# Kernel tuning notes

Measured on AMD Instinct MI355X. Metric: run time of the kernel, lower is better.

## Reference

```python
import jax, jax.numpy as jnp
import numpy as np

N, E = 50000, 800000
IN, H, C = 256, 8, 32  # heads=8, hidden_dim=32 -> out dim 256
NEG_SLOPE = 0.2
EPS = 1e-5


def setup_inputs() -> dict:
    key = jax.random.key(0)
    ks = jax.random.split(key, 6)
    x = jax.random.normal(ks[0], (N, IN), jnp.float32)
    edge_index = jax.random.randint(ks[1], (2, E), 0, N, dtype=jnp.int32)
    W = jax.random.normal(ks[2], (IN, H * C), jnp.float32) / np.sqrt(IN).astype(np.float32)
    att_src = jax.random.normal(ks[3], (H, C), jnp.float32) * 0.1
    att_dst = jax.random.normal(ks[4], (H, C), jnp.float32) * 0.1
    bias = jnp.zeros((H * C,), jnp.float32)
    gamma = jnp.ones((H * C,), jnp.float32)
    beta = jnp.zeros((H * C,), jnp.float32)
    return {"x": x, "edge_index": edge_index, "W": W, "att_src": att_src,
            "att_dst": att_dst, "bias": bias, "gamma": gamma, "beta": beta}


def reference(x, edge_index, W, att_src, att_dst, bias, gamma, beta):
    n = x.shape[0]
    # Linear projection -> per-head features [N, H, C]
    xl = (x @ W).reshape(n, H, C)
    # Per-node attention half-logits [N, H]
    a_src = jnp.einsum('nhc,hc->nh', xl, att_src)
    a_dst = jnp.einsum('nhc,hc->nh', xl, att_dst)
    # Add self loops (PyG GATConv default)
    loops = jnp.arange(n, dtype=edge_index.dtype)
    src = jnp.concatenate([edge_index[0], loops])  # [E+N]
    dst = jnp.concatenate([edge_index[1], loops])
    # Edge attention logits + segment softmax over destination neighborhoods
    logits = jax.nn.leaky_relu(a_src[src] + a_dst[dst], NEG_SLOPE)  # [E+N, H]
    seg_max = jax.ops.segment_max(logits, dst, num_segments=n)
    ex = jnp.exp(logits - seg_max[dst])
    denom = jax.ops.segment_sum(ex, dst, num_segments=n)
    alpha = ex / denom[dst]  # [E+N, H]
    # Weighted scatter-aggregation of source features
    msgs = xl[src] * alpha[:, :, None]  # [E+N, H, C]
    out = jax.ops.segment_sum(msgs, dst, num_segments=n).reshape(n, H * C) + bias
    # LayerNorm over feature dim
    mu = jnp.mean(out, axis=-1, keepdims=True)
    var = jnp.var(out, axis=-1, keepdims=True)
    return (out - mu) / jnp.sqrt(var + EPS) * gamma + beta
```

## Files before the change

### kernel.cpp

```cpp
#include <hip/hip_runtime.h>
#include <math.h>

#define NEG 0.2f
#define LNEPS 1e-5f

typedef __attribute__((ext_vector_type(8))) short bf16x8;
typedef __attribute__((ext_vector_type(4))) float f32x4;

__device__ __forceinline__ float lrelu(float x){ return x > 0.f ? x : NEG*x; }

__device__ __forceinline__ short f2b(float f){
  unsigned u = __float_as_uint(f);
  unsigned r = u + 0x7fffu + ((u >> 16) & 1u);
  return (short)(r >> 16);
}
__device__ __forceinline__ float b2f(unsigned short u){
  return __uint_as_float(((unsigned)u) << 16);
}

__global__ __launch_bounds__(256) void wt_k(const float* __restrict__ W,
                                            unsigned short* __restrict__ WT){
  int idx = blockIdx.x*256 + threadIdx.x;
  int k = idx >> 8, c = idx & 255;
  WT[c*256 + k] = (unsigned short)f2b(W[idx]);
}

__device__ __forceinline__ void load_half(float4 nx[8], const float* p){
  #pragma unroll
  for (int s=0;s<4;s++){
    nx[2*s]   = *(const float4*)(p + s*32);
    nx[2*s+1] = *(const float4*)(p + s*32 + 4);
  }
}
__device__ __forceinline__ void cvt_half(bf16x8 af[4], const float4 nx[8]){
  #pragma unroll
  for (int s=0;s<4;s++){
    af[s][0]=f2b(nx[2*s].x);   af[s][1]=f2b(nx[2*s].y);
    af[s][2]=f2b(nx[2*s].z);   af[s][3]=f2b(nx[2*s].w);
    af[s][4]=f2b(nx[2*s+1].x); af[s][5]=f2b(nx[2*s+1].y);
    af[s][6]=f2b(nx[2*s+1].z); af[s][7]=f2b(nx[2*s+1].w);
  }
}

__global__ __launch_bounds__(256, 2) void mfma_gemm_k(const float* __restrict__ A,
    const unsigned short* __restrict__ WT, unsigned short* __restrict__ Cb,
    const float* __restrict__ att_src, const float* __restrict__ att_dst,
    float* __restrict__ a_src, float* __restrict__ a_dst, int M, int nTiles){
  int w   = threadIdx.x >> 6;
  int l   = threadIdx.x & 63;
  int l15 = l & 15;
  int kg  = l >> 4;
  int colbase = w*64;

  bf16x8 bfr[4][8];
  #pragma unroll
  for (int j=0;j<4;j++){
    const unsigned short* bp = WT + (size_t)(colbase + j*16 + l15)*256 + kg*8;
    #pragma unroll
    for (int ks=0;ks<8;ks++) bfr[j][ks] = *(const bf16x8*)(bp + ks*32);
  }
  float as_r[4], ad_r[4];
  #pragma unroll
  for (int j=0;j<4;j++){
    as_r[j] = att_src[colbase + j*16 + l15];
    ad_r[j] = att_dst[colbase + j*16 + l15];
  }

  int t = blockIdx.x;
  if (t >= nTiles) return;
  int row0 = t*16 + l15;
  const float* ap = A + (size_t)(row0 < M ? row0 : M-1)*256 + kg*8;
  float4 nx[8];
  load_half(nx, ap);

  while (t < nTiles){
    f32x4 acc[4];
    #pragma unroll
    for (int j=0;j<4;j++) acc[j] = (f32x4){0.f,0.f,0.f,0.f};
    bf16x8 af[4];

    cvt_half(af, nx);
    load_half(nx, ap + 128);
    #pragma unroll
    for (int s=0;s<4;s++)
      #pragma unroll
      for (int j=0;j<4;j++)
        acc[j] = __builtin_amdgcn_mfma_f32_16x16x32_bf16(af[s], bfr[j][s], acc[j], 0, 0, 0);

    int tn = t + gridDim.x;
    int rown = tn < nTiles ? tn*16 + l15 : row0;
    const float* apn = A + (size_t)(rown < M ? rown : M-1)*256 + kg*8;

    cvt_half(af, nx);
    load_half(nx, apn);
    #pragma unroll
    for (int s=0;s<4;s++)
      #pragma unroll
      for (int j=0;j<4;j++)
        acc[j] = __builtin_amdgcn_mfma_f32_16x16x32_bf16(af[s], bfr[j][4+s], acc[j], 0, 0, 0);

    int orow_base = t*16 + kg*4;
    #pragma unroll
    for (int j=0;j<4;j++)
      #pragma unroll
      for (int rr=0;rr<4;rr++){
        int orow = orow_base + rr;
        if (orow < M) Cb[(size_t)orow*256 + colbase + j*16 + l15] = (unsigned short)f2b(acc[j][rr]);
      }
    #pragma unroll
    for (int rr=0;rr<4;rr++){
      float p0s = acc[0][rr]*as_r[0] + acc[1][rr]*as_r[1];
      float p0d = acc[0][rr]*ad_r[0] + acc[1][rr]*ad_r[1];
      float p1s = acc[2][rr]*as_r[2] + acc[3][rr]*as_r[3];
      float p1d = acc[2][rr]*ad_r[2] + acc[3][rr]*ad_r[3];
      #pragma unroll
      for (int m=1;m<16;m<<=1){
        p0s += __shfl_xor(p0s,m); p0d += __shfl_xor(p0d,m);
        p1s += __shfl_xor(p1s,m); p1d += __shfl_xor(p1d,m);
      }
      int orow = orow_base + rr;
      if (l15==0 && orow < M){
        a_src[(size_t)orow*8 + 2*w]   = p0s;
        a_dst[(size_t)orow*8 + 2*w]   = p0d;
        a_src[(size_t)orow*8 + 2*w+1] = p1s;
        a_dst[(size_t)orow*8 + 2*w+1] = p1d;
      }
    }
    t = tn; row0 = rown; ap = apn;
  }
}

__global__ void deg_k(const int* __restrict__ dst, int* __restrict__ deg, int E){
  int e = blockIdx.x*blockDim.x+threadIdx.x;
  if (e<E) atomicAdd(&deg[dst[e]],1);
}

__global__ __launch_bounds__(1024) void scan1_k(const int* __restrict__ deg,
                                                int* __restrict__ off,
                                                int* __restrict__ bsum, int n){
  __shared__ int wsum[16];
  int tid=threadIdx.x, lane=tid&63, wid=tid>>6;
  int i = blockIdx.x*1024 + tid;
  int v = (i<n)?deg[i]:0;
  int x = v;
  #pragma unroll
  for (int s=1;s<64;s<<=1){ int t2=__shfl_up(x,s); if (lane>=s) x+=t2; }
  if (lane==63) wsum[wid]=x;
  __syncthreads();
  if (tid<16){
    int y=wsum[tid];
    #pragma unroll
    for (int s=1;s<16;s<<=1){ int t2=__shfl_up(y,s); if (tid>=s) y+=t2; }
    wsum[tid]=y;
  }
  __syncthreads();
  int prefix=(wid? wsum[wid-1]:0);
  if (i<n) off[i]=prefix + x - v;
  if (tid==0) bsum[blockIdx.x]=wsum[15];
}

__global__ void scan2_k(int* __restrict__ bsum, int nb, int* __restrict__ offn){
  int lane = threadIdx.x;
  int v = (lane<nb)?bsum[lane]:0;
  int x = v;
  #pragma unroll
  for (int s=1;s<64;s<<=1){ int t2=__shfl_up(x,s); if (lane>=s) x+=t2; }
  if (lane<nb) bsum[lane] = x - v;
  if (lane==63) *offn = x;
}

__global__ __launch_bounds__(1024) void scan3_k(int* __restrict__ off,
                                                const int* __restrict__ bsum, int n){
  int i = blockIdx.x*1024 + threadIdx.x;
  if (i<n) off[i] += bsum[blockIdx.x];
}

__global__ void scatter_k(const int* __restrict__ src, const int* __restrict__ dst,
                          const int* __restrict__ off, int* __restrict__ cur,
                          int* __restrict__ sorted, int E){
  int e=blockIdx.x*blockDim.x+threadIdx.x;
  if (e<E){
    int d=dst[e];
    int pos=off[d]+atomicAdd(&cur[d],1);
    sorted[pos]=src[e];
  }
}

__global__ __launch_bounds__(256) void agg2_k(const unsigned short* __restrict__ xlb,
    const float* __restrict__ a_src, const float* __restrict__ a_dst,
    const int* __restrict__ off, const int* __restrict__ sorted,
    const float* __restrict__ bias, const float* __restrict__ gamma,
    const float* __restrict__ beta, float* __restrict__ out, int n){
  int node = blockIdx.x*4 + (threadIdx.x>>6);
  int lane = threadIdx.x & 63;
  if (node >= n) return;
  int h = lane >> 3;
  float myadst = a_dst[(size_t)node*8+h];
  int s0=off[node], d=off[node+1]-s0;

  float wgt = __expf(lrelu(a_src[(size_t)node*8+h]+myadst));
  float den = wgt;
  ushort4 u0 = *(const ushort4*)(xlb + (size_t)node*256 + lane*4);
  float ax=wgt*b2f(u0.x), ay=wgt*b2f(u0.y), az=wgt*b2f(u0.z), aw=wgt*b2f(u0.w);

  int i=0;
  for (; i+8<=d; i+=8){
    int s[8];
    #pragma unroll
    for (int j=0;j<8;j++) s[j] = sorted[s0+i+j];
    ushort4 u[8];
    #pragma unroll
    for (int j=0;j<8;j++) u[j] = *(const ushort4*)(xlb + (size_t)s[j]*256 + lane*4);
    float wv[8];
    #pragma unroll
    for (int j=0;j<8;j++) wv[j] = __expf(lrelu(a_src[(size_t)s[j]*8+h]+myadst));
    #pragma unroll
    for (int j=0;j<8;j++){
      den += wv[j];
      ax += wv[j]*b2f(u[j].x);
      ay += wv[j]*b2f(u[j].y);
      az += wv[j]*b2f(u[j].z);
      aw += wv[j]*b2f(u[j].w);
    }
  }
  for (; i<d; i++){
    int s1 = sorted[s0+i];
    float w1 = __expf(lrelu(a_src[(size_t)s1*8+h]+myadst));
    ushort4 u1 = *(const ushort4*)(xlb + (size_t)s1*256 + lane*4);
    den += w1;
    ax += w1*b2f(u1.x); ay += w1*b2f(u1.y); az += w1*b2f(u1.z); aw += w1*b2f(u1.w);
  }

  float rd = 1.0f/den;
  float4 b4 = *(const float4*)(bias + lane*4);
  float4 o = {ax*rd+b4.x, ay*rd+b4.y, az*rd+b4.z, aw*rd+b4.w};

  float sum = o.x+o.y+o.z+o.w;
  float ssq = o.x*o.x+o.y*o.y+o.z*o.z+o.w*o.w;
  #pragma unroll
  for (int s=1;s<64;s<<=1){ sum += __shfl_xor(sum,s); ssq += __shfl_xor(ssq,s); }
  float mean = sum*(1.0f/256.0f);
  float var  = ssq*(1.0f/256.0f) - mean*mean;
  float rstd = rsqrtf(var + LNEPS);
  float4 g  = *(const float4*)(gamma + lane*4);
  float4 be = *(const float4*)(beta + lane*4);
  o.x = (o.x-mean)*rstd*g.x+be.x;
  o.y = (o.y-mean)*rstd*g.y+be.y;
  o.z = (o.z-mean)*rstd*g.z+be.z;
  o.w = (o.w-mean)*rstd*g.w+be.w;
  *(float4*)(out + (size_t)node*256 + lane*4) = o;
}

extern "C" void kernel_launch(void* const* d_in, const int* in_sizes, int n_in,
                              void* d_out, int out_size, void* d_ws, size_t ws_size,
                              hipStream_t stream){
  const float* x       = (const float*)d_in[0];
  const int*   ei      = (const int*)  d_in[1];
  const float* W       = (const float*)d_in[2];
  const float* att_src = (const float*)d_in[3];
  const float* att_dst = (const float*)d_in[4];
  const float* bias    = (const float*)d_in[5];
  const float* gamma   = (const float*)d_in[6];
  const float* beta    = (const float*)d_in[7];
  float* out = (float*)d_out;

  int N = in_sizes[0]/256;
  int E = in_sizes[1]/2;
  const int* srcp = ei;
  const int* dstp = ei + E;

  unsigned short* xlb = (unsigned short*)d_ws;
  float* a_src = (float*)(xlb + (size_t)N*256);
  float* a_dst = a_src + (size_t)N*8;
  int*   deg   = (int*)(a_dst + (size_t)N*8);
  int*   off   = deg + N;
  int*   cur   = off + N + 1;
  int*   sorted= cur + N;
  int*   bsum  = sorted + E;
  unsigned short* WT = (unsigned short*)(bsum + 1024);

  hipMemsetAsync(deg, 0, (size_t)N*sizeof(int), stream);
  hipMemsetAsync(cur, 0, (size_t)N*sizeof(int), stream);

  int nb = (N + 1023)/1024;
  int nTiles = (N + 15)/16;

  wt_k<<<256, 256, 0, stream>>>(W, WT);
  mfma_gemm_k<<<512, 256, 0, stream>>>(x, WT, xlb, att_src, att_dst, a_src, a_dst, N, nTiles);
  deg_k<<<(E+255)/256, 256, 0, stream>>>(dstp, deg, E);
  scan1_k<<<nb, 1024, 0, stream>>>(deg, off, bsum, N);
  scan2_k<<<1, 64, 0, stream>>>(bsum, nb, off + N);
  scan3_k<<<nb, 1024, 0, stream>>>(off, bsum, N);
  scatter_k<<<(E+255)/256, 256, 0, stream>>>(srcp, dstp, off, cur, sorted, E);
  agg2_k<<<(N+3)/4, 256, 0, stream>>>(xlb, a_src, a_dst, off, sorted, bias, gamma, beta, out, N);
}
```

Before: 218.9 us.

## Split wavefront into two half-waves gathering 16-byte rows, fold self-loops into CSR

The aggregation kernel now has each half of a 64-lane wavefront process alternate neighbor edges. Each lane loads 8 bf16 values (16 bytes) per source row instead of 4, and the two halves are combined with a cross-half shuffle before the LayerNorm. Self loops are now inserted as CSR entries by a new kernel that initializes degree to 1 and places each node first in its segment, which replaces the two memsets and the special-cased self term. The intent is to keep more independent row gathers in flight with wider loads, at the cost of two extra small kernel launches and more registers per lane.

Result: faster. 209.7 us (-4.2%).

```diff
diff --git a/kernel.cpp b/kernel.cpp
--- a/kernel.cpp
+++ b/kernel.cpp
@@ -5,6 +5,7 @@
 #define LNEPS 1e-5f
 
 typedef __attribute__((ext_vector_type(8))) short bf16x8;
+typedef __attribute__((ext_vector_type(8))) unsigned short u16x8;
 typedef __attribute__((ext_vector_type(4))) float f32x4;
 
 __device__ __forceinline__ float lrelu(float x){ return x > 0.f ? x : NEG*x; }
@@ -130,6 +131,11 @@
   }
 }
 
+__global__ void dinit_k(int* __restrict__ deg, int n){
+  int i = blockIdx.x*blockDim.x+threadIdx.x;
+  if (i<n) deg[i]=1;
+}
+
 __global__ void deg_k(const int* __restrict__ dst, int* __restrict__ deg, int E){
   int e = blockIdx.x*blockDim.x+threadIdx.x;
   if (e<E) atomicAdd(&deg[dst[e]],1);
@@ -175,6 +181,12 @@
   if (i<n) off[i] += bsum[blockIdx.x];
 }
 
+__global__ void self_k(const int* __restrict__ off, int* __restrict__ sorted,
+                       int* __restrict__ cur, int n){
+  int i = blockIdx.x*blockDim.x+threadIdx.x;
+  if (i<n){ sorted[off[i]] = i; cur[i] = 1; }
+}
+
 __global__ void scatter_k(const int* __restrict__ src, const int* __restrict__ dst,
                           const int* __restrict__ off, int* __restrict__ cur,
                           int* __restrict__ sorted, int E){
@@ -186,69 +198,82 @@
   }
 }
 
-__global__ __launch_bounds__(256) void agg2_k(const unsigned short* __restrict__ xlb,
+__global__ __launch_bounds__(256) void agg3_k(const unsigned short* __restrict__ xlb,
     const float* __restrict__ a_src, const float* __restrict__ a_dst,
     const int* __restrict__ off, const int* __restrict__ sorted,
     const float* __restrict__ bias, const float* __restrict__ gamma,
     const float* __restrict__ beta, float* __restrict__ out, int n){
   int node = blockIdx.x*4 + (threadIdx.x>>6);
+  if (node >= n) return;
   int lane = threadIdx.x & 63;
-  if (node >= n) return;
-  int h = lane >> 3;
-  float myadst = a_dst[(size_t)node*8+h];
-  int s0=off[node], d=off[node+1]-s0;
-
-  float wgt = __expf(lrelu(a_src[(size_t)node*8+h]+myadst));
-  float den = wgt;
-  ushort4 u0 = *(const ushort4*)(xlb + (size_t)node*256 + lane*4);
-  float ax=wgt*b2f(u0.x), ay=wgt*b2f(u0.y), az=wgt*b2f(u0.z), aw=wgt*b2f(u0.w);
-
-  int i=0;
-  for (; i+8<=d; i+=8){
-    int s[8];
-    #pragma unroll
-    for (int j=0;j<8;j++) s[j] = sorted[s0+i+j];
-    ushort4 u[8];
-    #pragma unroll
-    for (int j=0;j<8;j++) u[j] = *(const ushort4*)(xlb + (size_t)s[j]*256 + lane*4);
-    float wv[8];
-    #pragma unroll
-    for (int j=0;j<8;j++) wv[j] = __expf(lrelu(a_src[(size_t)s[j]*8+h]+myadst));
-    #pragma unroll
-    for (int j=0;j<8;j++){
+  int half = lane >> 5;
+  int sl   = lane & 31;
+  int h    = sl >> 2;
+  float adst = a_dst[(size_t)node*8 + h];
+  int s0 = off[node], dd = off[node+1] - s0;
+
+  float acc[8] = {0.f,0.f,0.f,0.f,0.f,0.f,0.f,0.f};
+  float den = 0.f;
+
+  int i = 0;
+  for (; i+8 <= dd; i += 8){
+    int s[4];
+    #pragma unroll
+    for (int j=0;j<4;j++) s[j] = sorted[s0 + i + 2*j + half];
+    u16x8 u[4];
+    #pragma unroll
+    for (int j=0;j<4;j++) u[j] = *(const u16x8*)(xlb + (size_t)s[j]*256 + sl*8);
+    float wv[4];
+    #pragma unroll
+    for (int j=0;j<4;j++) wv[j] = __expf(lrelu(a_src[(size_t)s[j]*8+h]+adst));
+    #pragma unroll
+    for (int j=0;j<4;j++){
       den += wv[j];
-      ax += wv[j]*b2f(u[j].x);
-      ay += wv[j]*b2f(u[j].y);
-      az += wv[j]*b2f(u[j].z);
-      aw += wv[j]*b2f(u[j].w);
+      #pragma unroll
+      for (int k=0;k<8;k++) acc[k] += wv[j]*b2f((unsigned short)u[j][k]);
     }
   }
-  for (; i<d; i++){
-    int s1 = sorted[s0+i];
-    float w1 = __expf(lrelu(a_src[(size_t)s1*8+h]+myadst));
-    ushort4 u1 = *(const ushort4*)(xlb + (size_t)s1*256 + lane*4);
+  for (; i < dd; i += 2){
+    int idx = i + half;
+    bool ok = idx < dd;
+    int s1 = ok ? sorted[s0+idx] : node;
+    u16x8 u1 = *(const u16x8*)(xlb + (size_t)s1*256 + sl*8);
+    float w1 = ok ? __expf(lrelu(a_src[(size_t)s1*8+h]+adst)) : 0.f;
     den += w1;
-    ax += w1*b2f(u1.x); ay += w1*b2f(u1.y); az += w1*b2f(u1.z); aw += w1*b2f(u1.w);
-  }
+    #pragma unroll
+    for (int k=0;k<8;k++) acc[k] += w1*b2f((unsigned short)u1[k]);
+  }
+
+  den += __shfl_xor(den, 32);
+  #pragma unroll
+  for (int k=0;k<8;k++) acc[k] += __shfl_xor(acc[k], 32);
 
   float rd = 1.0f/den;
-  float4 b4 = *(const float4*)(bias + lane*4);
-  float4 o = {ax*rd+b4.x, ay*rd+b4.y, az*rd+b4.z, aw*rd+b4.w};
-
-  float sum = o.x+o.y+o.z+o.w;
-  float ssq = o.x*o.x+o.y*o.y+o.z*o.z+o.w*o.w;
-  #pragma unroll
-  for (int s=1;s<64;s<<=1){ sum += __shfl_xor(sum,s); ssq += __shfl_xor(ssq,s); }
+  float4 bia0 = *(const float4*)(bias + sl*8);
+  float4 bia1 = *(const float4*)(bias + sl*8 + 4);
+  float o[8];
+  o[0]=acc[0]*rd+bia0.x; o[1]=acc[1]*rd+bia0.y; o[2]=acc[2]*rd+bia0.z; o[3]=acc[3]*rd+bia0.w;
+  o[4]=acc[4]*rd+bia1.x; o[5]=acc[5]*rd+bia1.y; o[6]=acc[6]*rd+bia1.z; o[7]=acc[7]*rd+bia1.w;
+
+  float sum=0.f, ssq=0.f;
+  #pragma unroll
+  for (int k=0;k<8;k++){ sum += o[k]; ssq += o[k]*o[k]; }
+  #pragma unroll
+  for (int s=1;s<32;s<<=1){ sum += __shfl_xor(sum,s); ssq += __shfl_xor(ssq,s); }
   float mean = sum*(1.0f/256.0f);
   float var  = ssq*(1.0f/256.0f) - mean*mean;
   float rstd = rsqrtf(var + LNEPS);
-  float4 g  = *(const float4*)(gamma + lane*4);
-  float4 be = *(const float4*)(beta + lane*4);
-  o.x = (o.x-mean)*rstd*g.x+be.x;
-  o.y = (o.y-mean)*rstd*g.y+be.y;
-  o.z = (o.z-mean)*rstd*g.z+be.z;
-  o.w = (o.w-mean)*rstd*g.w+be.w;
-  *(float4*)(out + (size_t)node*256 + lane*4) = o;
+
+  int f = sl*8 + half*4;
+  float4 g  = *(const float4*)(gamma + f);
+  float4 be = *(const float4*)(beta + f);
+  int kb = half*4;
+  float4 ov;
+  ov.x = (o[kb+0]-mean)*rstd*g.x+be.x;
+  ov.y = (o[kb+1]-mean)*rstd*g.y+be.y;
+  ov.z = (o[kb+2]-mean)*rstd*g.z+be.z;
+  ov.w = (o[kb+3]-mean)*rstd*g.w+be.w;
+  *(float4*)(out + (size_t)node*256 + f) = ov;
 }
 
 extern "C" void kernel_launch(void* const* d_in, const int* in_sizes, int n_in,
@@ -276,21 +301,20 @@
   int*   off   = deg + N;
   int*   cur   = off + N + 1;
   int*   sorted= cur + N;
-  int*   bsum  = sorted + E;
+  int*   bsum  = sorted + E + N;
   unsigned short* WT = (unsigned short*)(bsum + 1024);
-
-  hipMemsetAsync(deg, 0, (size_t)N*sizeof(int), stream);
-  hipMemsetAsync(cur, 0, (size_t)N*sizeof(int), stream);
 
   int nb = (N + 1023)/1024;
   int nTiles = (N + 15)/16;
 
   wt_k<<<256, 256, 0, stream>>>(W, WT);
   mfma_gemm_k<<<512, 256, 0, stream>>>(x, WT, xlb, att_src, att_dst, a_src, a_dst, N, nTiles);
+  dinit_k<<<(N+255)/256, 256, 0, stream>>>(deg, N);
   deg_k<<<(E+255)/256, 256, 0, stream>>>(dstp, deg, E);
   scan1_k<<<nb, 1024, 0, stream>>>(deg, off, bsum, N);
   scan2_k<<<1, 64, 0, stream>>>(bsum, nb, off + N);
   scan3_k<<<nb, 1024, 0, stream>>>(off, bsum, N);
+  self_k<<<(N+255)/256, 256, 0, stream>>>(off, sorted, cur, N);
   scatter_k<<<(E+255)/256, 256, 0, stream>>>(srcp, dstp, off, cur, sorted, E);
-  agg2_k<<<(N+3)/4, 256, 0, stream>>>(xlb, a_src, a_dst, off, sorted, bias, gamma, beta, out, N);
-}
+  agg3_k<<<(N+3)/4, 256, 0, stream>>>(xlb, a_src, a_dst, off, sorted, bias, gamma, beta, out, N);
+}
```
